# Kernel tuning notes

Hardware: AMD Instinct MI355X
Metric: run time of the kernel (lower is better)

## Reference

```python
import math
import jax, jax.numpy as jnp
import numpy as np
from jax import lax

EPS = 1e-5


def setup_inputs() -> dict:
    key = jax.random.key(0)
    ks = jax.random.split(key, 12)
    B, L, C = 4, 4096, 512
    d_inner, d_state, d_conv = 2 * C, 4, 4
    dt_rank = math.ceil(C / 16)  # 32
    s = 0.02
    A = jnp.tile(jnp.arange(1, d_state + 1, dtype=jnp.float32), (d_inner, 1))
    return {
        "hidden_states": jax.random.normal(ks[0], (B, L, C), jnp.float32),
        "mask": jnp.zeros((B, L), jnp.int32),
        "residual": jax.random.normal(ks[1], (B, L, C), jnp.float32),
        "norm_weight": jnp.ones((C,), jnp.float32),
        "conv_w": jax.random.normal(ks[2], (C, C, 3, 3), jnp.float32) * s,
        "conv_b": jnp.zeros((C,), jnp.float32),
        "in_proj_w": jax.random.normal(ks[3], (2 * d_inner, C), jnp.float32) * s,
        "conv1d_w": jax.random.normal(ks[4], (d_inner, 1, d_conv), jnp.float32) * s,
        "conv1d_b": jnp.zeros((d_inner,), jnp.float32),
        "x_proj_w": jax.random.normal(ks[5], (dt_rank + 2 * d_state, d_inner), jnp.float32) * s,
        "dt_proj_w": jax.random.normal(ks[6], (d_inner, dt_rank), jnp.float32) * s,
        "dt_proj_b": jnp.full((d_inner,), -4.6, jnp.float32),  # softplus ~ 0.01
        "A_log": jnp.log(A),
        "D": jnp.ones((d_inner,), jnp.float32),
        "out_proj_w": jax.random.normal(ks[7], (C, 2 * C), jnp.float32) * s,
    }


def _mamba(u, in_proj_w, conv1d_w, conv1d_b, x_proj_w, dt_proj_w, dt_proj_b, A_log, D, out_proj_w):
    # u: [B, L, C]
    Bn, Ln, _ = u.shape
    d_inner = conv1d_w.shape[0]
    d_state = A_log.shape[1]
    dt_rank = dt_proj_w.shape[1]
    d_conv = conv1d_w.shape[-1]
    xz = jnp.einsum("blc,ec->ble", u, in_proj_w)  # [B,L,2*d_inner]
    x, z = jnp.split(xz, 2, axis=-1)
    # causal depthwise conv1d (left pad d_conv-1)
    xc = lax.conv_general_dilated(
        x.transpose(0, 2, 1), conv1d_w, (1,), ((d_conv - 1, 0),),
        feature_group_count=d_inner, dimension_numbers=("NCH", "OIH", "NCH"))
    x = jax.nn.silu((xc + conv1d_b[None, :, None]).transpose(0, 2, 1))  # [B,L,D]
    x_dbl = jnp.einsum("bld,ed->ble", x, x_proj_w)
    dtr, Bm, Cm = jnp.split(x_dbl, [dt_rank, dt_rank + d_state], axis=-1)
    dt = jax.nn.softplus(jnp.einsum("blr,dr->bld", dtr, dt_proj_w) + dt_proj_b)
    A = -jnp.exp(A_log)  # [D,N]
    dA = jnp.exp(dt[..., None] * A)                              # [B,L,D,N]
    dBx = dt[..., None] * Bm[:, :, None, :] * x[..., None]       # [B,L,D,N]

    def step(h, t):
        dA_t, dBx_t, C_t = t
        h = dA_t * h + dBx_t
        return h, jnp.einsum("bdn,bn->bd", h, C_t)

    h0 = jnp.zeros((Bn, d_inner, d_state), dt.dtype)
    _, ys = lax.scan(step, h0, (dA.transpose(1, 0, 2, 3), dBx.transpose(1, 0, 2, 3), Cm.transpose(1, 0, 2)))
    y = ys.transpose(1, 0, 2) + x * D
    y = y * jax.nn.silu(z)
    return jnp.einsum("bld,cd->blc", y, out_proj_w)


def reference(hidden_states, mask, residual, norm_weight, conv_w, conv_b,
              in_proj_w, conv1d_w, conv1d_b, x_proj_w, dt_proj_w, dt_proj_b,
              A_log, D, out_proj_w):
    # fused add + RMSNorm, prenorm, residual in fp32
    res = (hidden_states + residual).astype(jnp.float32)
    var = jnp.mean(res * res, axis=-1, keepdims=True)
    hs = res * lax.rsqrt(var + EPS) * norm_weight
    Bn, Ln, Cn = hs.shape
    Ls = int(round(math.sqrt(Ln)))
    img = hs.transpose(0, 2, 1).reshape(Bn, Cn, Ls, Ls)
    img = lax.conv_general_dilated(img, conv_w, (1, 1), ((1, 1), (1, 1)),
                                   dimension_numbers=("NCHW", "OIHW", "NCHW"))
    img = img + conv_b[None, :, None, None]
    hs = img.reshape(Bn, Cn, Ln).transpose(0, 2, 1)  # [B,L,C]
    # gather tokens where mask==0 (equal count per row; here n_easy = L)
    n_easy = Ln
    order = jnp.argsort(mask, axis=1, stable=True)
    easy_idx = order[:, :n_easy]  # [B, n_easy]
    easy = jnp.take_along_axis(hs, easy_idx[:, :, None], axis=1)
    mixed = _mamba(easy, in_proj_w, conv1d_w, conv1d_b, x_proj_w,
                   dt_proj_w, dt_proj_b, A_log, D, out_proj_w)
    # scatter mixer output back into the full sequence
    x = hs.at[jnp.arange(Bn)[:, None], easy_idx].set(mixed)
    return x, res
```

## Files before the change

### kernel.cpp

```cpp
#include <hip/hip_runtime.h>
#include <hip/hip_bf16.h>

#define BB 4
#define LL 4096
#define CC 512
#define DI 1024
#define DS 4
#define DR 32
#define LS 64
#define CHUNK 64
#define NCH 64
#define PW 66

typedef unsigned short ushortT;
typedef __attribute__((ext_vector_type(8))) short bf16x8;
typedef __attribute__((ext_vector_type(4))) float f32x4;

static __device__ __forceinline__ float b2f(ushortT u) {
    union { unsigned int i; float f; } v; v.i = ((unsigned int)u) << 16; return v.f;
}
static __device__ __forceinline__ ushortT f2b(float f) {
    unsigned int x = __float_as_uint(f);
    unsigned int lsb = (x >> 16) & 1u;
    x += 0x7fffu + lsb;
    return (ushortT)(x >> 16);
}

static __device__ __forceinline__ void gl16(const ushortT* g, ushortT* l) {
    typedef const __attribute__((address_space(1))) unsigned int GU;
    typedef __attribute__((address_space(3))) unsigned int LU;
    __builtin_amdgcn_global_load_lds((GU*)(unsigned long long)(const void*)g,
                                     (LU*)(unsigned int)(unsigned long long)(void*)l,
                                     16, 0, 0);
}

__global__ __launch_bounds__(128) void k_norm(const float* __restrict__ hid,
                                              const float* __restrict__ resi,
                                              const float* __restrict__ nw,
                                              float* __restrict__ out_res,
                                              ushortT* __restrict__ himg) {
    int bl = blockIdx.x;
    int t  = threadIdx.x;
    size_t base = (size_t)bl * CC;
    float4 hv = ((const float4*)(hid + base))[t];
    float4 rv = ((const float4*)(resi + base))[t];
    float4 h = { hv.x + rv.x, hv.y + rv.y, hv.z + rv.z, hv.w + rv.w };
    ((float4*)(out_res + base))[t] = h;

    float s = h.x * h.x + h.y * h.y + h.z * h.z + h.w * h.w;
    #pragma unroll
    for (int o = 32; o > 0; o >>= 1) s += __shfl_xor(s, o);
    __shared__ float ws[2];
    if ((t & 63) == 0) ws[t >> 6] = s;
    __syncthreads();
    float scale = rsqrtf((ws[0] + ws[1]) / (float)CC + 1e-5f);

    float4 nv = ((const float4*)nw)[t];
    int b = bl >> 12, l = bl & 4095;
    int iy = (l >> 6) + 1, ix = (l & 63) + 1;
    ushort4 o4 = { f2b(h.x * scale * nv.x), f2b(h.y * scale * nv.y),
                   f2b(h.z * scale * nv.z), f2b(h.w * scale * nv.w) };
    ((ushort4*)(himg + (((size_t)b * PW + iy) * PW + ix) * CC))[t] = o4;
}

__global__ __launch_bounds__(256) void k_prep1(const float* __restrict__ convw,
                                               const float* __restrict__ inw,
                                               ushortT* __restrict__ wb3,
                                               ushortT* __restrict__ wbi) {
    int blk = blockIdx.x, tid = threadIdx.x;
    if (blk < 1024) {
        int g = blk * 256 + tid;
        int ic = g & 511, oc = g >> 9;
        const float* src = convw + ((size_t)(oc * CC + ic)) * 9;
        #pragma unroll
        for (int tap = 0; tap < 9; tap++)
            wb3[((size_t)oc * 9 + tap) * 512 + ic] = f2b(src[tap]);
    } else {
        int i = (blk - 1024) * 256 + tid;
        float4 v = ((const float4*)inw)[i];
        ushort4 o = { f2b(v.x), f2b(v.y), f2b(v.z), f2b(v.w) };
        ((ushort4*)wbi)[i] = o;
    }
}

__global__ __launch_bounds__(256) void k_prep2(const float* __restrict__ outw,
                                               const float* __restrict__ xpw,
                                               const float* __restrict__ dtw,
                                               ushortT* __restrict__ wbo,
                                               ushortT* __restrict__ wbx,
                                               ushortT* __restrict__ dtwb) {
    int blk = blockIdx.x, tid = threadIdx.x;
    if (blk < 512) {
        int i = blk * 256 + tid;
        float4 v = ((const float4*)outw)[i];
        ushort4 o = { f2b(v.x), f2b(v.y), f2b(v.z), f2b(v.w) };
        ((ushort4*)wbo)[i] = o;
    } else if (blk < 768) {
        int g = (blk - 512) * 256 + tid;
        int k = g & 1023, e = g >> 10;
        wbx[g] = (e < 40) ? f2b(xpw[(size_t)e * DI + k]) : (ushortT)0;
    } else {
        int i = (blk - 768) * 256 + tid;
        float4 v = ((const float4*)dtw)[i];
        ushort4 o = { f2b(v.x), f2b(v.y), f2b(v.z), f2b(v.w) };
        ((ushort4*)dtwb)[i] = o;
    }
}

__global__ __launch_bounds__(256) void k_conv2d_mfma(const ushortT* __restrict__ himg,
                                                     const ushortT* __restrict__ wb3,
                                                     const float* __restrict__ convb,
                                                     ushortT* __restrict__ u) {
    const int b = blockIdx.z;
    const int ytile = blockIdx.x;
    const int n0 = blockIdx.y * 128;
    const int tid = threadIdx.x;
    const int lane = tid & 63, w = tid >> 6;
    const int wr = w >> 1, wc = w & 1;
    const int fm = lane & 15, kg = lane >> 4;

    __shared__ __align__(16) ushortT As[128][64];
    __shared__ __align__(16) ushortT Bs[128][64];

    f32x4 acc[4][4];
    #pragma unroll
    for (int i = 0; i < 4; i++)
        #pragma unroll
        for (int j = 0; j < 4; j++) acc[i][j] = (f32x4){0.f, 0.f, 0.f, 0.f};

    const int sp8 = lane >> 3;
    const int sch = ((lane & 7) ^ sp8) * 8;

    for (int tap = 0; tap < 9; tap++) {
        const int dy = tap / 3 - 1, dx = tap % 3 - 1;
        size_t ag[4], bg[4];
        #pragma unroll
        for (int j = 0; j < 4; j++) {
            int p  = w * 32 + j * 8 + sp8;
            int iy = ytile * 2 + (p >> 6) + dy + 1;
            int ix = (p & 63) + dx + 1;
            ag[j] = (((size_t)b * PW + iy) * PW + ix) * CC + sch;
            bg[j] = ((size_t)(n0 + p) * 9 + tap) * 512 + sch;
        }
        for (int ics = 0; ics < 8; ics++) {
            const int ko = ics * 64;
            #pragma unroll
            for (int j = 0; j < 4; j++) {
                gl16(himg + ag[j] + ko, &As[w * 32 + j * 8][0]);
                gl16(wb3  + bg[j] + ko, &Bs[w * 32 + j * 8][0]);
            }
            __syncthreads();
            #pragma unroll
            for (int ks = 0; ks < 2; ks++) {
                const int rc = ((ks * 4 + kg) ^ (fm & 7)) * 8;
                bf16x8 afr[4], bfr[4];
                #pragma unroll
                for (int ms = 0; ms < 4; ms++)
                    afr[ms] = *(const bf16x8*)(&As[wr * 64 + ms * 16 + fm][rc]);
                #pragma unroll
                for (int ns = 0; ns < 4; ns++)
                    bfr[ns] = *(const bf16x8*)(&Bs[wc * 64 + ns * 16 + fm][rc]);
                #pragma unroll
                for (int ms = 0; ms < 4; ms++)
                    #pragma unroll
                    for (int ns = 0; ns < 4; ns++)
                        acc[ms][ns] = __builtin_amdgcn_mfma_f32_16x16x32_bf16(afr[ms], bfr[ns], acc[ms][ns], 0, 0, 0);
            }
            __syncthreads();
        }
    }

    const int rowb = ytile * 128 + wr * 64;
    const int colb = n0 + wc * 64;
    #pragma unroll
    for (int ms = 0; ms < 4; ms++) {
        #pragma unroll
        for (int ns = 0; ns < 4; ns++) {
            int col = colb + ns * 16 + fm;
            float bias = convb[col];
            f32x4 v = acc[ms][ns];
            #pragma unroll
            for (int r = 0; r < 4; r++) {
                int row = rowb + ms * 16 + kg * 4 + r;
                u[((size_t)(b * LL + row)) * CC + col] = f2b(v[r] + bias);
            }
        }
    }
}

__global__ __launch_bounds__(256) void k_inproj_mfma(const ushortT* __restrict__ A,
                                                     const ushortT* __restrict__ Wb,
                                                     ushortT* __restrict__ xout,
                                                     ushortT* __restrict__ zout) {
    const int m0 = blockIdx.x * 128, n0 = blockIdx.y * 128;
    const int tid = threadIdx.x;
    const int lane = tid & 63, w = tid >> 6;
    const int wr = w >> 1, wc = w & 1;
    const int fm = lane & 15, kg = lane >> 4;

    __shared__ __align__(16) ushortT As[128][64];
    __shared__ __align__(16) ushortT Bs[128][64];

    f32x4 acc[4][4];
    #pragma unroll
    for (int i = 0; i < 4; i++)
        #pragma unroll
        for (int j = 0; j < 4; j++) acc[i][j] = (f32x4){0.f, 0.f, 0.f, 0.f};

    const int sp8 = lane >> 3;
    const int sch = ((lane & 7) ^ sp8) * 8;

    for (int k0 = 0; k0 < CC; k0 += 64) {
        #pragma unroll
        for (int j = 0; j < 4; j++) {
            int p = w * 32 + j * 8 + sp8;
            gl16(A  + (size_t)(m0 + p) * CC + k0 + sch, &As[w * 32 + j * 8][0]);
            gl16(Wb + (size_t)(n0 + p) * CC + k0 + sch, &Bs[w * 32 + j * 8][0]);
        }
        __syncthreads();
        #pragma unroll
        for (int ks = 0; ks < 2; ks++) {
            const int rc = ((ks * 4 + kg) ^ (fm & 7)) * 8;
            bf16x8 afr[4], bfr[4];
            #pragma unroll
            for (int ms = 0; ms < 4; ms++)
                afr[ms] = *(const bf16x8*)(&As[wr * 64 + ms * 16 + fm][rc]);
            #pragma unroll
            for (int ns = 0; ns < 4; ns++)
                bfr[ns] = *(const bf16x8*)(&Bs[wc * 64 + ns * 16 + fm][rc]);
            #pragma unroll
            for (int ms = 0; ms < 4; ms++)
                #pragma unroll
                for (int ns = 0; ns < 4; ns++)
                    acc[ms][ns] = __builtin_amdgcn_mfma_f32_16x16x32_bf16(afr[ms], bfr[ns], acc[ms][ns], 0, 0, 0);
        }
        __syncthreads();
    }

    const int rowb = m0 + wr * 64;
    const int colb = n0 + wc * 64;
    #pragma unroll
    for (int ms = 0; ms < 4; ms++) {
        #pragma unroll
        for (int ns = 0; ns < 4; ns++) {
            int col = colb + ns * 16 + fm;
            f32x4 v = acc[ms][ns];
            #pragma unroll
            for (int r = 0; r < 4; r++) {
                int row = rowb + ms * 16 + kg * 4 + r;
                float val = v[r];
                if (col < DI) {
                    xout[(size_t)row * DI + col] = f2b(val);
                } else {
                    float s = val / (1.f + __expf(-val));
                    zout[(size_t)row * DI + (col - DI)] = f2b(s);
                }
            }
        }
    }
}

__global__ __launch_bounds__(256) void k_outproj_mfma(const ushortT* __restrict__ A,
                                                      const ushortT* __restrict__ Wb,
                                                      float* __restrict__ out) {
    const int m0 = blockIdx.x * 128, n0 = blockIdx.y * 128;
    const int tid = threadIdx.x;
    const int lane = tid & 63, w = tid >> 6;
    const int wr = w >> 1, wc = w & 1;
    const int fm = lane & 15, kg = lane >> 4;

    __shared__ __align__(16) ushortT As[128][64];
    __shared__ __align__(16) ushortT Bs[128][64];

    f32x4 acc[4][4];
    #pragma unroll
    for (int i = 0; i < 4; i++)
        #pragma unroll
        for (int j = 0; j < 4; j++) acc[i][j] = (f32x4){0.f, 0.f, 0.f, 0.f};

    const int sp8 = lane >> 3;
    const int sch = ((lane & 7) ^ sp8) * 8;

    for (int k0 = 0; k0 < DI; k0 += 64) {
        #pragma unroll
        for (int j = 0; j < 4; j++) {
            int p = w * 32 + j * 8 + sp8;
            gl16(A  + (size_t)(m0 + p) * DI + k0 + sch, &As[w * 32 + j * 8][0]);
            gl16(Wb + (size_t)(n0 + p) * DI + k0 + sch, &Bs[w * 32 + j * 8][0]);
        }
        __syncthreads();
        #pragma unroll
        for (int ks = 0; ks < 2; ks++) {
            const int rc = ((ks * 4 + kg) ^ (fm & 7)) * 8;
            bf16x8 afr[4], bfr[4];
            #pragma unroll
            for (int ms = 0; ms < 4; ms++)
                afr[ms] = *(const bf16x8*)(&As[wr * 64 + ms * 16 + fm][rc]);
            #pragma unroll
            for (int ns = 0; ns < 4; ns++)
                bfr[ns] = *(const bf16x8*)(&Bs[wc * 64 + ns * 16 + fm][rc]);
            #pragma unroll
            for (int ms = 0; ms < 4; ms++)
                #pragma unroll
                for (int ns = 0; ns < 4; ns++)
                    acc[ms][ns] = __builtin_amdgcn_mfma_f32_16x16x32_bf16(afr[ms], bfr[ns], acc[ms][ns], 0, 0, 0);
        }
        __syncthreads();
    }

    const int rowb = m0 + wr * 64;
    const int colb = n0 + wc * 64;
    #pragma unroll
    for (int ms = 0; ms < 4; ms++) {
        #pragma unroll
        for (int ns = 0; ns < 4; ns++) {
            int col = colb + ns * 16 + fm;
            f32x4 v = acc[ms][ns];
            #pragma unroll
            for (int r = 0; r < 4; r++) {
                int row = rowb + ms * 16 + kg * 4 + r;
                out[(size_t)row * CC + col] = v[r];
            }
        }
    }
}

__global__ __launch_bounds__(256) void k_xproj_mfma(const ushortT* __restrict__ A,
                                                    const ushortT* __restrict__ Wb,
                                                    float* __restrict__ xdbl,
                                                    ushortT* __restrict__ dtr_b) {
    const int m0 = blockIdx.x * 64;
    const int tid = threadIdx.x;
    const int lane = tid & 63, w = tid >> 6;
    const int fm = lane & 15, kg = lane >> 4;

    __shared__ __align__(16) ushortT As[64][32];
    __shared__ __align__(16) ushortT Bs[64][32];

    f32x4 acc[4];
    #pragma unroll
    for (int j = 0; j < 4; j++) acc[j] = (f32x4){0.f, 0.f, 0.f, 0.f};

    const int sp  = lane >> 2;
    const int sch = (((lane & 3) ^ ((sp >> 1) & 3))) * 8;
    const int rc  = (kg ^ ((fm >> 1) & 3)) * 8;

    for (int k0 = 0; k0 < DI; k0 += 32) {
        gl16(A  + (size_t)(m0 + w * 16 + sp) * DI + k0 + sch, &As[w * 16][0]);
        gl16(Wb + (size_t)(w * 16 + sp) * DI + k0 + sch, &Bs[w * 16][0]);
        __syncthreads();
        bf16x8 afr = *(const bf16x8*)(&As[w * 16 + fm][rc]);
        bf16x8 bfr[4];
        #pragma unroll
        for (int ns = 0; ns < 4; ns++)
            bfr[ns] = *(const bf16x8*)(&Bs[ns * 16 + fm][rc]);
        #pragma unroll
        for (int ns = 0; ns < 4; ns++)
            acc[ns] = __builtin_amdgcn_mfma_f32_16x16x32_bf16(afr, bfr[ns], acc[ns], 0, 0, 0);
        __syncthreads();
    }

    #pragma unroll
    for (int ns = 0; ns < 4; ns++) {
        int col = ns * 16 + fm;
        f32x4 v = acc[ns];
        #pragma unroll
        for (int r = 0; r < 4; r++) {
            int row = m0 + w * 16 + kg * 4 + r;
            float val = v[r];
            if (col < 40) xdbl[(size_t)row * 40 + col] = val;
            if (col < 32) dtr_b[(size_t)row * 32 + col] = f2b(val);
        }
    }
}

__global__ __launch_bounds__(256) void k_dt_mfma(const ushortT* __restrict__ Ab,
                                                 const ushortT* __restrict__ Wb,
                                                 const float* __restrict__ dtb,
                                                 ushortT* __restrict__ dty) {
    const int m0 = blockIdx.x * 128, n0 = blockIdx.y * 128;
    const int tid = threadIdx.x;
    const int lane = tid & 63, w = tid >> 6;
    const int wr = w >> 1, wc = w & 1;
    const int fm = lane & 15, kg = lane >> 4;

    __shared__ ushortT As[128][40];
    __shared__ ushortT Bs[128][40];

    f32x4 acc[4][4];
    #pragma unroll
    for (int i = 0; i < 4; i++)
        #pragma unroll
        for (int j = 0; j < 4; j++) acc[i][j] = (f32x4){0.f, 0.f, 0.f, 0.f};

    const int ar = tid >> 2;
    const int lcol = (tid & 3) * 8;
    #pragma unroll
    for (int q = 0; q < 2; q++) {
        int r = ar + q * 64;
        bf16x8 av = *(const bf16x8*)(Ab + (size_t)(m0 + r) * 32 + lcol);
        bf16x8 bv = *(const bf16x8*)(Wb + (size_t)(n0 + r) * 32 + lcol);
        *(bf16x8*)(&As[r][lcol]) = av;
        *(bf16x8*)(&Bs[r][lcol]) = bv;
    }
    __syncthreads();
    bf16x8 afr[4], bfr[4];
    #pragma unroll
    for (int ms = 0; ms < 4; ms++)
        afr[ms] = *(const bf16x8*)(&As[wr * 64 + ms * 16 + fm][kg * 8]);
    #pragma unroll
    for (int ns = 0; ns < 4; ns++)
        bfr[ns] = *(const bf16x8*)(&Bs[wc * 64 + ns * 16 + fm][kg * 8]);
    #pragma unroll
    for (int ms = 0; ms < 4; ms++)
        #pragma unroll
        for (int ns = 0; ns < 4; ns++)
            acc[ms][ns] = __builtin_amdgcn_mfma_f32_16x16x32_bf16(afr[ms], bfr[ns], acc[ms][ns], 0, 0, 0);

    const int rowb = m0 + wr * 64;
    const int colb = n0 + wc * 64;
    #pragma unroll
    for (int ms = 0; ms < 4; ms++) {
        #pragma unroll
        for (int ns = 0; ns < 4; ns++) {
            int col = colb + ns * 16 + fm;
            float bias = dtb[col];
            f32x4 v = acc[ms][ns];
            #pragma unroll
            for (int r = 0; r < 4; r++) {
                int row = rowb + ms * 16 + kg * 4 + r;
                float a = v[r] + bias;
                float sp = (a > 20.f) ? a : log1pf(__expf(a));
                dty[(size_t)row * DI + col] = f2b(sp);
            }
        }
    }
}

__global__ __launch_bounds__(256) void k_conv1d(const ushortT* __restrict__ xbuf,
                                                const float* __restrict__ w,
                                                const float* __restrict__ bias,
                                                ushortT* __restrict__ xs) {
    int g = blockIdx.x * 256 + threadIdx.x;
    int d8 = g & 127;
    int l  = (g >> 7) & (LL - 1);
    int b  = g >> 19;
    int d0 = d8 * 8;

    float wreg[32];
    {
        const float4* wp = (const float4*)(w + d0 * 4);
        #pragma unroll
        for (int q = 0; q < 8; q++) {
            float4 v = wp[q];
            wreg[q * 4 + 0] = v.x; wreg[q * 4 + 1] = v.y;
            wreg[q * 4 + 2] = v.z; wreg[q * 4 + 3] = v.w;
        }
    }
    float acc[8];
    {
        float4 b0 = *(const float4*)(bias + d0);
        float4 b1 = *(const float4*)(bias + d0 + 4);
        acc[0] = b0.x; acc[1] = b0.y; acc[2] = b0.z; acc[3] = b0.w;
        acc[4] = b1.x; acc[5] = b1.y; acc[6] = b1.z; acc[7] = b1.w;
    }
    #pragma unroll
    for (int k = 0; k < 4; k++) {
        int ll = l + k - 3;
        if (ll >= 0) {
            bf16x8 v = *(const bf16x8*)(xbuf + ((size_t)(b * LL + ll)) * DI + d0);
            #pragma unroll
            for (int j = 0; j < 8; j++)
                acc[j] += b2f((ushortT)v[j]) * wreg[j * 4 + k];
        }
    }
    bf16x8 o;
    #pragma unroll
    for (int j = 0; j < 8; j++) {
        float s = acc[j] / (1.f + __expf(-acc[j]));
        o[j] = (short)f2b(s);
    }
    *(bf16x8*)(xs + ((size_t)(b * LL + l)) * DI + d0) = o;
}

__global__ __launch_bounds__(256) void k_scan_p1(const ushortT* __restrict__ dt,
                                                 const ushortT* __restrict__ xs,
                                                 const float* __restrict__ xdbl,
                                                 const float* __restrict__ alog,
                                                 float* __restrict__ P,
                                                 float* __restrict__ S) {
    int d0 = (blockIdx.x * 256 + threadIdx.x) * 2;
    int ch = blockIdx.y;
    int b  = blockIdx.z;
    int t  = threadIdx.x;

    __shared__ float sB[CHUNK][4];
    if (t < CHUNK) {
        const float* xr = xdbl + ((size_t)(b * LL + ch * CHUNK + t)) * 40;
        float4 v = *(const float4*)(xr + 32);
        sB[t][0] = v.x; sB[t][1] = v.y; sB[t][2] = v.z; sB[t][3] = v.w;
    }
    __syncthreads();

    float An[2][4], h[2][4] = {}, Pp[2][4];
    #pragma unroll
    for (int e = 0; e < 2; e++)
        #pragma unroll
        for (int n = 0; n < 4; n++) {
            An[e][n] = -__expf(alog[(d0 + e) * 4 + n]);
            Pp[e][n] = 1.f;
        }

    size_t row0 = (size_t)b * LL + ch * CHUNK;
    for (int i = 0; i < CHUNK; i++) {
        size_t row = row0 + i;
        ushort2 dv = *(const ushort2*)(dt + row * DI + d0);
        ushort2 xv = *(const ushort2*)(xs + row * DI + d0);
        float dtv[2] = { b2f(dv.x), b2f(dv.y) };
        float dbx[2] = { dtv[0] * b2f(xv.x), dtv[1] * b2f(xv.y) };
        #pragma unroll
        for (int e = 0; e < 2; e++)
            #pragma unroll
            for (int n = 0; n < 4; n++) {
                float dA = __expf(dtv[e] * An[e][n]);
                h[e][n]  = dA * h[e][n] + dbx[e] * sB[i][n];
                Pp[e][n] *= dA;
            }
    }
    #pragma unroll
    for (int e = 0; e < 2; e++) {
        size_t o = (((size_t)b * NCH + ch) * DI + d0 + e) * 4;
        *(float4*)(P + o) = make_float4(Pp[e][0], Pp[e][1], Pp[e][2], Pp[e][3]);
        *(float4*)(S + o) = make_float4(h[e][0], h[e][1], h[e][2], h[e][3]);
    }
}

__global__ __launch_bounds__(256) void k_scan_cmb(const float* __restrict__ P,
                                                  const float* __restrict__ S,
                                                  float* __restrict__ Hin) {
    int td = blockIdx.x * 256 + threadIdx.x;
    int b = td >> 10, d = td & (DI - 1);
    float h[4] = {0.f, 0.f, 0.f, 0.f};
    for (int ch = 0; ch < NCH; ch++) {
        size_t o = (((size_t)b * NCH + ch) * DI + d) * 4;
        *(float4*)(Hin + o) = make_float4(h[0], h[1], h[2], h[3]);
        float4 p = *(const float4*)(P + o);
        float4 s = *(const float4*)(S + o);
        h[0] = p.x * h[0] + s.x;
        h[1] = p.y * h[1] + s.y;
        h[2] = p.z * h[2] + s.z;
        h[3] = p.w * h[3] + s.w;
    }
}

__global__ __launch_bounds__(256) void k_scan_p2(ushortT* dty,
                                                 const ushortT* __restrict__ xs,
                                                 const float* __restrict__ xdbl,
                                                 const ushortT* __restrict__ zs,
                                                 const float* __restrict__ alog,
                                                 const float* __restrict__ Dv,
                                                 const float* __restrict__ Hin) {
    int d0 = (blockIdx.x * 256 + threadIdx.x) * 2;
    int ch = blockIdx.y;
    int b  = blockIdx.z;
    int t  = threadIdx.x;

    __shared__ float sBC[CHUNK][8];
    if (t < CHUNK) {
        const float* xr = xdbl + ((size_t)(b * LL + ch * CHUNK + t)) * 40;
        float4 v1 = *(const float4*)(xr + 32);
        float4 v2 = *(const float4*)(xr + 36);
        sBC[t][0] = v1.x; sBC[t][1] = v1.y; sBC[t][2] = v1.z; sBC[t][3] = v1.w;
        sBC[t][4] = v2.x; sBC[t][5] = v2.y; sBC[t][6] = v2.z; sBC[t][7] = v2.w;
    }
    __syncthreads();

    float An[2][4], h[2][4], Dd[2];
    #pragma unroll
    for (int e = 0; e < 2; e++) {
        #pragma unroll
        for (int n = 0; n < 4; n++)
            An[e][n] = -__expf(alog[(d0 + e) * 4 + n]);
        Dd[e] = Dv[d0 + e];
        size_t o = (((size_t)b * NCH + ch) * DI + d0 + e) * 4;
        float4 h0 = *(const float4*)(Hin + o);
        h[e][0] = h0.x; h[e][1] = h0.y; h[e][2] = h0.z; h[e][3] = h0.w;
    }

    size_t row0 = (size_t)b * LL + ch * CHUNK;
    for (int i = 0; i < CHUNK; i++) {
        size_t row = row0 + i;
        ushort2 dv = *(const ushort2*)(dty + row * DI + d0);
        ushort2 xv = *(const ushort2*)(xs  + row * DI + d0);
        ushort2 zv = *(const ushort2*)(zs  + row * DI + d0);
        float dtv[2] = { b2f(dv.x), b2f(dv.y) };
        float xvf[2] = { b2f(xv.x), b2f(xv.y) };
        float out[2];
        #pragma unroll
        for (int e = 0; e < 2; e++) {
            float dbx = dtv[e] * xvf[e];
            float y = 0.f;
            #pragma unroll
            for (int n = 0; n < 4; n++) {
                float dA = __expf(dtv[e] * An[e][n]);
                h[e][n] = dA * h[e][n] + dbx * sBC[i][n];
                y += h[e][n] * sBC[i][4 + n];
            }
            float sz = b2f((e == 0) ? zv.x : zv.y);
            out[e] = (y + xvf[e] * Dd[e]) * sz;
        }
        ushort2 o2 = { f2b(out[0]), f2b(out[1]) };
        *(ushort2*)(dty + row * DI + d0) = o2;
    }
}

__global__ __launch_bounds__(256) void k_sentinel(float* __restrict__ out0) {
    int i = blockIdx.x * 256 + threadIdx.x;
    out0[i] = 1.0f;
}

extern "C" void kernel_launch(void* const* d_in, const int* in_sizes, int n_in,
                              void* d_out, int out_size, void* d_ws, size_t ws_size,
                              hipStream_t stream) {
    const float* hid   = (const float*)d_in[0];
    const float* resi  = (const float*)d_in[2];
    const float* nw    = (const float*)d_in[3];
    const float* convw = (const float*)d_in[4];
    const float* convb = (const float*)d_in[5];
    const float* inw   = (const float*)d_in[6];
    const float* c1w   = (const float*)d_in[7];
    const float* c1b   = (const float*)d_in[8];
    const float* xpw   = (const float*)d_in[9];
    const float* dtw   = (const float*)d_in[10];
    const float* dtb   = (const float*)d_in[11];
    const float* alog  = (const float*)d_in[12];
    const float* Dv    = (const float*)d_in[13];
    const float* outw  = (const float*)d_in[14];

    float* out0 = (float*)d_out;
    float* out1 = out0 + (size_t)BB * LL * CC;

    const size_t RA = (size_t)BB * LL * CC * 2;
    const size_t RB = (size_t)BB * LL * DI * 2;
    const size_t NEED = RA + 2 * RB;
    const size_t HIMG_BYTES = (size_t)BB * PW * PW * CC * 2;

    ushortT* himg  = (ushortT*)d_out;
    ushortT* wbi   = (ushortT*)((char*)d_out + (18u << 20));
    ushortT* xs    = (ushortT*)d_out;
    char* base = (char*)d_ws;
    ushortT* u     = (ushortT*)base;
    float*   xdbl  = (float*)base;
    ushortT* wbx   = (ushortT*)(base + 2621440);
    ushortT* dtwb  = (ushortT*)(base + 2752512);
    ushortT* wbo   = (ushortT*)(base + (3u << 20));
    float*   Pbuf  = (float*)(base + (4u << 20));
    ushortT* dtr_b = (ushortT*)(base + (4u << 20));
    float*   Sbuf  = (float*)(base + (8u << 20));
    float*   Hin   = (float*)(base + (12u << 20));
    ushortT* wb3   = (ushortT*)(base + RA);
    ushortT* xb    = (ushortT*)(base + RA);
    ushortT* dty   = (ushortT*)(base + RA);
    ushortT* zsilu = (ushortT*)(base + RA + RB);

    if (ws_size < NEED) {
        k_sentinel<<<(BB * LL * CC) / 256, 256, 0, stream>>>(out0);
        return;
    }

    hipMemsetAsync(himg, 0, HIMG_BYTES, stream);
    k_norm<<<BB * LL, 128, 0, stream>>>(hid, resi, nw, out1, himg);
    k_prep1<<<2048, 256, 0, stream>>>(convw, inw, wb3, wbi);
    k_conv2d_mfma<<<dim3(32, 4, BB), 256, 0, stream>>>(himg, wb3, convb, u);
    k_inproj_mfma<<<dim3(128, 16), 256, 0, stream>>>(u, wbi, xb, zsilu);
    k_prep2<<<800, 256, 0, stream>>>(outw, xpw, dtw, wbo, wbx, dtwb);
    k_conv1d<<<8192, 256, 0, stream>>>(xb, c1w, c1b, xs);
    k_xproj_mfma<<<256, 256, 0, stream>>>(xs, wbx, xdbl, dtr_b);
    k_dt_mfma<<<dim3(128, 8), 256, 0, stream>>>(dtr_b, dtwb, dtb, dty);
    k_scan_p1<<<dim3(2, NCH, BB), 256, 0, stream>>>(dty, xs, xdbl, alog, Pbuf, Sbuf);
    k_scan_cmb<<<(BB * DI) / 256, 256, 0, stream>>>(Pbuf, Sbuf, Hin);
    k_scan_p2<<<dim3(2, NCH, BB), 256, 0, stream>>>(dty, xs, xdbl, zsilu, alog, Dv, Hin);
    k_outproj_mfma<<<dim3(128, 4), 256, 0, stream>>>(dty, wbo, out0);
}
```

Before: 394.8 us.

## Fuse dt projection and softplus into both scan passes, drop dt materialization

Removes the separate dt-projection MFMA kernel and the 8 MB bf16 dt tensor. Each scan thread now recomputes dt for its channel from the 32-wide dt_rank vector held in shared memory and 32 dt_proj weights held in registers, then applies softplus. x_proj writes only the B/C columns to a compact buffer. Threads now own one channel each with 512-thread blocks. This trades dt memory traffic and one launch for a 32-term dot product that runs twice per element.

```diff
diff --git a/kernel.cpp b/kernel.cpp
--- a/kernel.cpp
+++ b/kernel.cpp
@@ -85,25 +85,18 @@
 
 __global__ __launch_bounds__(256) void k_prep2(const float* __restrict__ outw,
                                                const float* __restrict__ xpw,
-                                               const float* __restrict__ dtw,
                                                ushortT* __restrict__ wbo,
-                                               ushortT* __restrict__ wbx,
-                                               ushortT* __restrict__ dtwb) {
+                                               ushortT* __restrict__ wbx) {
     int blk = blockIdx.x, tid = threadIdx.x;
     if (blk < 512) {
         int i = blk * 256 + tid;
         float4 v = ((const float4*)outw)[i];
         ushort4 o = { f2b(v.x), f2b(v.y), f2b(v.z), f2b(v.w) };
         ((ushort4*)wbo)[i] = o;
-    } else if (blk < 768) {
+    } else {
         int g = (blk - 512) * 256 + tid;
         int k = g & 1023, e = g >> 10;
         wbx[g] = (e < 40) ? f2b(xpw[(size_t)e * DI + k]) : (ushortT)0;
-    } else {
-        int i = (blk - 768) * 256 + tid;
-        float4 v = ((const float4*)dtw)[i];
-        ushort4 o = { f2b(v.x), f2b(v.y), f2b(v.z), f2b(v.w) };
-        ((ushort4*)dtwb)[i] = o;
     }
 }
 
@@ -327,7 +320,7 @@
 
 __global__ __launch_bounds__(256) void k_xproj_mfma(const ushortT* __restrict__ A,
                                                     const ushortT* __restrict__ Wb,
-                                                    float* __restrict__ xdbl,
+                                                    float* __restrict__ bcbuf,
                                                     ushortT* __restrict__ dtr_b) {
     const int m0 = blockIdx.x * 64;
     const int tid = threadIdx.x;
@@ -368,71 +361,8 @@
         for (int r = 0; r < 4; r++) {
             int row = m0 + w * 16 + kg * 4 + r;
             float val = v[r];
-            if (col < 40) xdbl[(size_t)row * 40 + col] = val;
             if (col < 32) dtr_b[(size_t)row * 32 + col] = f2b(val);
-        }
-    }
-}
-
-__global__ __launch_bounds__(256) void k_dt_mfma(const ushortT* __restrict__ Ab,
-                                                 const ushortT* __restrict__ Wb,
-                                                 const float* __restrict__ dtb,
-                                                 ushortT* __restrict__ dty) {
-    const int m0 = blockIdx.x * 128, n0 = blockIdx.y * 128;
-    const int tid = threadIdx.x;
-    const int lane = tid & 63, w = tid >> 6;
-    const int wr = w >> 1, wc = w & 1;
-    const int fm = lane & 15, kg = lane >> 4;
-
-    __shared__ ushortT As[128][40];
-    __shared__ ushortT Bs[128][40];
-
-    f32x4 acc[4][4];
-    #pragma unroll
-    for (int i = 0; i < 4; i++)
-        #pragma unroll
-        for (int j = 0; j < 4; j++) acc[i][j] = (f32x4){0.f, 0.f, 0.f, 0.f};
-
-    const int ar = tid >> 2;
-    const int lcol = (tid & 3) * 8;
-    #pragma unroll
-    for (int q = 0; q < 2; q++) {
-        int r = ar + q * 64;
-        bf16x8 av = *(const bf16x8*)(Ab + (size_t)(m0 + r) * 32 + lcol);
-        bf16x8 bv = *(const bf16x8*)(Wb + (size_t)(n0 + r) * 32 + lcol);
-        *(bf16x8*)(&As[r][lcol]) = av;
-        *(bf16x8*)(&Bs[r][lcol]) = bv;
-    }
-    __syncthreads();
-    bf16x8 afr[4], bfr[4];
-    #pragma unroll
-    for (int ms = 0; ms < 4; ms++)
-        afr[ms] = *(const bf16x8*)(&As[wr * 64 + ms * 16 + fm][kg * 8]);
-    #pragma unroll
-    for (int ns = 0; ns < 4; ns++)
-        bfr[ns] = *(const bf16x8*)(&Bs[wc * 64 + ns * 16 + fm][kg * 8]);
-    #pragma unroll
-    for (int ms = 0; ms < 4; ms++)
-        #pragma unroll
-        for (int ns = 0; ns < 4; ns++)
-            acc[ms][ns] = __builtin_amdgcn_mfma_f32_16x16x32_bf16(afr[ms], bfr[ns], acc[ms][ns], 0, 0, 0);
-
-    const int rowb = m0 + wr * 64;
-    const int colb = n0 + wc * 64;
-    #pragma unroll
-    for (int ms = 0; ms < 4; ms++) {
-        #pragma unroll
-        for (int ns = 0; ns < 4; ns++) {
-            int col = colb + ns * 16 + fm;
-            float bias = dtb[col];
-            f32x4 v = acc[ms][ns];
-            #pragma unroll
-            for (int r = 0; r < 4; r++) {
-                int row = rowb + ms * 16 + kg * 4 + r;
-                float a = v[r] + bias;
-                float sp = (a > 20.f) ? a : log1pf(__expf(a));
-                dty[(size_t)row * DI + col] = f2b(sp);
-            }
+            else if (col < 40) bcbuf[(size_t)row * 8 + (col - 32)] = val;
         }
     }
 }
@@ -483,56 +413,65 @@
     *(bf16x8*)(xs + ((size_t)(b * LL + l)) * DI + d0) = o;
 }
 
-__global__ __launch_bounds__(256) void k_scan_p1(const ushortT* __restrict__ dt,
+__global__ __launch_bounds__(512) void k_scan_p1(const ushortT* __restrict__ dtr_b,
                                                  const ushortT* __restrict__ xs,
-                                                 const float* __restrict__ xdbl,
+                                                 const float* __restrict__ bcbuf,
+                                                 const float* __restrict__ dtw,
+                                                 const float* __restrict__ dtb,
                                                  const float* __restrict__ alog,
                                                  float* __restrict__ P,
                                                  float* __restrict__ S) {
-    int d0 = (blockIdx.x * 256 + threadIdx.x) * 2;
+    int d  = blockIdx.x * 512 + threadIdx.x;
     int ch = blockIdx.y;
     int b  = blockIdx.z;
     int t  = threadIdx.x;
-
-    __shared__ float sB[CHUNK][4];
+    size_t row0 = (size_t)b * LL + ch * CHUNK;
+
+    __shared__ float   sB[CHUNK][4];
+    __shared__ ushortT sdtr[CHUNK][32];
+    {
+        int t4 = t * 4;
+        int r = t4 >> 5, off = t4 & 31;
+        *(ushort4*)(&sdtr[r][off]) = *(const ushort4*)(dtr_b + (row0 + r) * 32 + off);
+    }
     if (t < CHUNK) {
-        const float* xr = xdbl + ((size_t)(b * LL + ch * CHUNK + t)) * 40;
-        float4 v = *(const float4*)(xr + 32);
+        float4 v = *(const float4*)(bcbuf + (row0 + t) * 8);
         sB[t][0] = v.x; sB[t][1] = v.y; sB[t][2] = v.z; sB[t][3] = v.w;
     }
     __syncthreads();
 
-    float An[2][4], h[2][4] = {}, Pp[2][4];
-    #pragma unroll
-    for (int e = 0; e < 2; e++)
+    float dtwr[32];
+    {
+        const float4* wp = (const float4*)(dtw + d * 32);
+        #pragma unroll
+        for (int q = 0; q < 8; q++) {
+            float4 v = wp[q];
+            dtwr[q * 4 + 0] = v.x; dtwr[q * 4 + 1] = v.y;
+            dtwr[q * 4 + 2] = v.z; dtwr[q * 4 + 3] = v.w;
+        }
+    }
+    float dtbd = dtb[d];
+    float An[4], h[4] = {0.f, 0.f, 0.f, 0.f}, Pp[4] = {1.f, 1.f, 1.f, 1.f};
+    #pragma unroll
+    for (int n = 0; n < 4; n++) An[n] = -__expf(alog[d * 4 + n]);
+
+    for (int i = 0; i < CHUNK; i++) {
+        float a = dtbd;
+        #pragma unroll 8
+        for (int k = 0; k < 32; k++) a += b2f(sdtr[i][k]) * dtwr[k];
+        float dtv = (a > 20.f) ? a : log1pf(__expf(a));
+        float xv = b2f(xs[(row0 + i) * DI + d]);
+        float dbx = dtv * xv;
         #pragma unroll
         for (int n = 0; n < 4; n++) {
-            An[e][n] = -__expf(alog[(d0 + e) * 4 + n]);
-            Pp[e][n] = 1.f;
-        }
-
-    size_t row0 = (size_t)b * LL + ch * CHUNK;
-    for (int i = 0; i < CHUNK; i++) {
-        size_t row = row0 + i;
-        ushort2 dv = *(const ushort2*)(dt + row * DI + d0);
-        ushort2 xv = *(const ushort2*)(xs + row * DI + d0);
-        float dtv[2] = { b2f(dv.x), b2f(dv.y) };
-        float dbx[2] = { dtv[0] * b2f(xv.x), dtv[1] * b2f(xv.y) };
-        #pragma unroll
-        for (int e = 0; e < 2; e++)
-            #pragma unroll
-            for (int n = 0; n < 4; n++) {
-                float dA = __expf(dtv[e] * An[e][n]);
-                h[e][n]  = dA * h[e][n] + dbx[e] * sB[i][n];
-                Pp[e][n] *= dA;
-            }
-    }
-    #pragma unroll
-    for (int e = 0; e < 2; e++) {
-        size_t o = (((size_t)b * NCH + ch) * DI + d0 + e) * 4;
-        *(float4*)(P + o) = make_float4(Pp[e][0], Pp[e][1], Pp[e][2], Pp[e][3]);
-        *(float4*)(S + o) = make_float4(h[e][0], h[e][1], h[e][2], h[e][3]);
-    }
+            float dA = __expf(dtv * An[n]);
+            h[n]  = dA * h[n] + dbx * sB[i][n];
+            Pp[n] *= dA;
+        }
+    }
+    size_t o = (((size_t)b * NCH + ch) * DI + d) * 4;
+    *(float4*)(P + o) = make_float4(Pp[0], Pp[1], Pp[2], Pp[3]);
+    *(float4*)(S + o) = make_float4(h[0], h[1], h[2], h[3]);
 }
 
 __global__ __launch_bounds__(256) void k_scan_cmb(const float* __restrict__ P,
@@ -553,64 +492,74 @@
     }
 }
 
-__global__ __launch_bounds__(256) void k_scan_p2(ushortT* dty,
+__global__ __launch_bounds__(512) void k_scan_p2(const ushortT* __restrict__ dtr_b,
                                                  const ushortT* __restrict__ xs,
-                                                 const float* __restrict__ xdbl,
+                                                 const float* __restrict__ bcbuf,
                                                  const ushortT* __restrict__ zs,
+                                                 const float* __restrict__ dtw,
+                                                 const float* __restrict__ dtb,
                                                  const float* __restrict__ alog,
                                                  const float* __restrict__ Dv,
-                                                 const float* __restrict__ Hin) {
-    int d0 = (blockIdx.x * 256 + threadIdx.x) * 2;
+                                                 const float* __restrict__ Hin,
+                                                 ushortT* __restrict__ yout) {
+    int d  = blockIdx.x * 512 + threadIdx.x;
     int ch = blockIdx.y;
     int b  = blockIdx.z;
     int t  = threadIdx.x;
-
-    __shared__ float sBC[CHUNK][8];
+    size_t row0 = (size_t)b * LL + ch * CHUNK;
+
+    __shared__ float   sBC[CHUNK][8];
+    __shared__ ushortT sdtr[CHUNK][32];
+    {
+        int t4 = t * 4;
+        int r = t4 >> 5, off = t4 & 31;
+        *(ushort4*)(&sdtr[r][off]) = *(const ushort4*)(dtr_b + (row0 + r) * 32 + off);
+    }
     if (t < CHUNK) {
-        const float* xr = xdbl + ((size_t)(b * LL + ch * CHUNK + t)) * 40;
-        float4 v1 = *(const float4*)(xr + 32);
-        float4 v2 = *(const float4*)(xr + 36);
+        float4 v1 = *(const float4*)(bcbuf + (row0 + t) * 8);
+        float4 v2 = *(const float4*)(bcbuf + (row0 + t) * 8 + 4);
         sBC[t][0] = v1.x; sBC[t][1] = v1.y; sBC[t][2] = v1.z; sBC[t][3] = v1.w;
         sBC[t][4] = v2.x; sBC[t][5] = v2.y; sBC[t][6] = v2.z; sBC[t][7] = v2.w;
     }
     __syncthreads();
 
-    float An[2][4], h[2][4], Dd[2];
-    #pragma unroll
-    for (int e = 0; e < 2; e++) {
-        #pragma unroll
-        for (int n = 0; n < 4; n++)
-            An[e][n] = -__expf(alog[(d0 + e) * 4 + n]);
-        Dd[e] = Dv[d0 + e];
-        size_t o = (((size_t)b * NCH + ch) * DI + d0 + e) * 4;
-        float4 h0 = *(const float4*)(Hin + o);
-        h[e][0] = h0.x; h[e][1] = h0.y; h[e][2] = h0.z; h[e][3] = h0.w;
-    }
-
-    size_t row0 = (size_t)b * LL + ch * CHUNK;
+    float dtwr[32];
+    {
+        const float4* wp = (const float4*)(dtw + d * 32);
+        #pragma unroll
+        for (int q = 0; q < 8; q++) {
+            float4 v = wp[q];
+            dtwr[q * 4 + 0] = v.x; dtwr[q * 4 + 1] = v.y;
+            dtwr[q * 4 + 2] = v.z; dtwr[q * 4 + 3] = v.w;
+        }
+    }
+    float dtbd = dtb[d];
+    float An[4];
+    #pragma unroll
+    for (int n = 0; n < 4; n++) An[n] = -__expf(alog[d * 4 + n]);
+    float Dd = Dv[d];
+
+    size_t o = (((size_t)b * NCH + ch) * DI + d) * 4;
+    float4 h0 = *(const float4*)(Hin + o);
+    float h[4] = {h0.x, h0.y, h0.z, h0.w};
+
     for (int i = 0; i < CHUNK; i++) {
         size_t row = row0 + i;
-        ushort2 dv = *(const ushort2*)(dty + row * DI + d0);
-        ushort2 xv = *(const ushort2*)(xs  + row * DI + d0);
-        ushort2 zv = *(const ushort2*)(zs  + row * DI + d0);
-        float dtv[2] = { b2f(dv.x), b2f(dv.y) };
-        float xvf[2] = { b2f(xv.x), b2f(xv.y) };
-        float out[2];
-        #pragma unroll
-        for (int e = 0; e < 2; e++) {
-            float dbx = dtv[e] * xvf[e];
-            float y = 0.f;
-            #pragma unroll
-            for (int n = 0; n < 4; n++) {
-                float dA = __expf(dtv[e] * An[e][n]);
-                h[e][n] = dA * h[e][n] + dbx * sBC[i][n];
-                y += h[e][n] * sBC[i][4 + n];
-            }
-            float sz = b2f((e == 0) ? zv.x : zv.y);
-            out[e] = (y + xvf[e] * Dd[e]) * sz;
-        }
-        ushort2 o2 = { f2b(out[0]), f2b(out[1]) };
-        *(ushort2*)(dty + row * DI + d0) = o2;
+        float a = dtbd;
+        #pragma unroll 8
+        for (int k = 0; k < 32; k++) a += b2f(sdtr[i][k]) * dtwr[k];
+        float dtv = (a > 20.f) ? a : log1pf(__expf(a));
+        float xv = b2f(xs[row * DI + d]);
+        float dbx = dtv * xv;
+        float y = 0.f;
+        #pragma unroll
+        for (int n = 0; n < 4; n++) {
+            float dA = __expf(dtv * An[n]);
+            h[n] = dA * h[n] + dbx * sBC[i][n];
+            y += h[n] * sBC[i][4 + n];
+        }
+        float sz = b2f(zs[row * DI + d]);
+        yout[row * DI + d] = f2b((y + xv * Dd) * sz);
     }
 }
 
@@ -650,17 +599,16 @@
     ushortT* xs    = (ushortT*)d_out;
     char* base = (char*)d_ws;
     ushortT* u     = (ushortT*)base;
-    float*   xdbl  = (float*)base;
-    ushortT* wbx   = (ushortT*)(base + 2621440);
-    ushortT* dtwb  = (ushortT*)(base + 2752512);
-    ushortT* wbo   = (ushortT*)(base + (3u << 20));
-    float*   Pbuf  = (float*)(base + (4u << 20));
-    ushortT* dtr_b = (ushortT*)(base + (4u << 20));
-    float*   Sbuf  = (float*)(base + (8u << 20));
-    float*   Hin   = (float*)(base + (12u << 20));
+    float*   bcbuf = (float*)base;
+    ushortT* wbx   = (ushortT*)(base + 524288);
+    ushortT* wbo   = (ushortT*)(base + 655360);
+    ushortT* dtr_b = (ushortT*)(base + 1703936);
+    float*   Pbuf  = (float*)(base + 2752512);
+    float*   Sbuf  = (float*)(base + 6946816);
+    float*   Hin   = (float*)(base + 11141120);
     ushortT* wb3   = (ushortT*)(base + RA);
     ushortT* xb    = (ushortT*)(base + RA);
-    ushortT* dty   = (ushortT*)(base + RA);
+    ushortT* yb    = (ushortT*)(base + RA);
     ushortT* zsilu = (ushortT*)(base + RA + RB);
 
     if (ws_size < NEED) {
@@ -673,12 +621,11 @@
     k_prep1<<<2048, 256, 0, stream>>>(convw, inw, wb3, wbi);
     k_conv2d_mfma<<<dim3(32, 4, BB), 256, 0, stream>>>(himg, wb3, convb, u);
     k_inproj_mfma<<<dim3(128, 16), 256, 0, stream>>>(u, wbi, xb, zsilu);
-    k_prep2<<<800, 256, 0, stream>>>(outw, xpw, dtw, wbo, wbx, dtwb);
+    k_prep2<<<768, 256, 0, stream>>>(outw, xpw, wbo, wbx);
     k_conv1d<<<8192, 256, 0, stream>>>(xb, c1w, c1b, xs);
-    k_xproj_mfma<<<256, 256, 0, stream>>>(xs, wbx, xdbl, dtr_b);
-    k_dt_mfma<<<dim3(128, 8), 256, 0, stream>>>(dtr_b, dtwb, dtb, dty);
-    k_scan_p1<<<dim3(2, NCH, BB), 256, 0, stream>>>(dty, xs, xdbl, alog, Pbuf, Sbuf);
+    k_xproj_mfma<<<256, 256, 0, stream>>>(xs, wbx, bcbuf, dtr_b);
+    k_scan_p1<<<dim3(DI / 512, NCH, BB), 512, 0, stream>>>(dtr_b, xs, bcbuf, dtw, dtb, alog, Pbuf, Sbuf);
     k_scan_cmb<<<(BB * DI) / 256, 256, 0, stream>>>(Pbuf, Sbuf, Hin);
-    k_scan_p2<<<dim3(2, NCH, BB), 256, 0, stream>>>(dty, xs, xdbl, zsilu, alog, Dv, Hin);
-    k_outproj_mfma<<<dim3(128, 4), 256, 0, stream>>>(dty, wbo, out0);
-}
+    k_scan_p2<<<dim3(DI / 512, NCH, BB), 512, 0, stream>>>(dtr_b, xs, bcbuf, zsilu, dtw, dtb, alog, Dv, Hin, yb);
+    k_outproj_mfma<<<dim3(128, 4), 256, 0, stream>>>(yb, wbo, out0);
+}
```

Result: slower. 545.6 us (+38.2%).
